# Performance work log

Hardware: AMD Instinct MI355X
Metric: run time of the kernel (lower is better)

## Reference

```python
import jax, jax.numpy as jnp
import numpy as np

B, D, V, T = 256, 1024, 32000, 64  # num_seqs, hidden dim, vocab, history len


def setup_inputs() -> dict:
    key = jax.random.key(0)
    ks = jax.random.split(key, 8)
    hidden = jax.random.normal(ks[0], (B, D), dtype=jnp.float32)
    embedding = jax.random.normal(ks[1], (V, D), dtype=jnp.float32) * (1.0 / np.sqrt(D))
    output_tokens = jax.random.randint(ks[2], (B, T), 0, V, dtype=jnp.int64)
    presence_penalties = jax.random.uniform(ks[3], (B,), dtype=jnp.float32)
    frequency_penalties = jax.random.uniform(ks[4], (B,), dtype=jnp.float32)
    temperatures = jax.random.uniform(ks[5], (B,), dtype=jnp.float32) + 0.5  # > eps
    top_ps = jax.random.uniform(ks[6], (B,), dtype=jnp.float32) * 0.5 + 0.5  # in [0.5, 1.0)
    top_ks = jax.random.randint(ks[7], (B,), 1, V, dtype=jnp.int64)
    return {
        "hidden": hidden,
        "embedding": embedding,
        "output_tokens": output_tokens,
        "presence_penalties": presence_penalties,
        "frequency_penalties": frequency_penalties,
        "temperatures": temperatures,
        "top_ps": top_ps,
        "top_ks": top_ks,
    }


def reference(hidden, embedding, output_tokens, presence_penalties,
              frequency_penalties, temperatures, top_ps, top_ks):
    # 1) logits = pruned hidden states @ embedding^T  -> [B, V]
    logits = jnp.einsum("bd,vd->bv", hidden, embedding)
    b, v = logits.shape

    # 2) presence/frequency penalties via per-row token histogram (np.bincount equiv)
    rows = jnp.broadcast_to(jnp.arange(b)[:, None], output_tokens.shape)
    counts = jnp.zeros((b, v), logits.dtype).at[rows, output_tokens].add(1.0)
    logits = logits - frequency_penalties[:, None] * counts \
                    - presence_penalties[:, None] * (counts > 0).astype(logits.dtype)

    # 3) temperature scaling
    logits = logits / temperatures[:, None]

    # 4) probabilities
    probs = jax.nn.softmax(logits, axis=-1)

    # 5) top-p / top-k: descending sort, cumsum masks, scatter back via inverse perm
    order = jnp.argsort(-probs, axis=-1)                       # descending order
    probs_sort = jnp.take_along_axis(probs, order, axis=-1)
    probs_cum = jnp.cumsum(probs_sort, axis=-1)
    top_p_mask = (probs_cum - probs_sort) > top_ps[:, None]
    top_k_mask = jnp.arange(v)[None, :] >= top_ks[:, None]
    probs_sort = jnp.where(top_p_mask | top_k_mask, 0.0, probs_sort)
    inv = jnp.argsort(order, axis=-1)
    filtered_probs = jnp.take_along_axis(probs_sort, inv, axis=-1)  # original order
    return filtered_probs
```

## Files before the change

### kernel.cpp

```cpp
#include <hip/hip_runtime.h>
#include <math.h>

#define NB 256
#define NV 32000
#define ND 1024
#define NT 64

#define GN 64
#define BSTR 40
#define NKB 64
#define AKBF 8192
#define NGBLK (NV / GN)
#define INV2048F 4.8828125e-4f

#define NBIN 1024
#define HSTR 1032
#define HTOT (4 * HSTR)
#define FIX2 4294967296.0
#define SMASK ((1ull << 48) - 1ull)

typedef _Float16 f16x8 __attribute__((ext_vector_type(8)));
typedef _Float16 f16x4 __attribute__((ext_vector_type(4)));
typedef float f32x16 __attribute__((ext_vector_type(16)));

struct RowP2 {
  unsigned long long basePack;
  unsigned long long toppZfix;
  unsigned pfx;
  int ktop;
  float invZ;
  unsigned ustar;
  int m;
  int cEq;
};

__device__ __forceinline__ unsigned mono_enc(float f) {
  unsigned u = __float_as_uint(f);
  return (u & 0x80000000u) ? ~u : (u | 0x80000000u);
}
__device__ __forceinline__ float mono_dec(unsigned u) {
  return (u & 0x80000000u) ? __uint_as_float(u & 0x7FFFFFFFu) : __uint_as_float(~u);
}

__global__ __launch_bounds__(256) void convert_A(const float* __restrict__ hidden,
                                                 _Float16* __restrict__ A3,
                                                 unsigned* __restrict__ rowmax) {
  if (blockIdx.x == 0) rowmax[threadIdx.x] = 0u;
  const int g = blockIdx.x * 256 + threadIdx.x;
  const int kb = g >> 10, rem = g & 1023, r = rem >> 2, c = rem & 3;
  const float4 a4 = *(const float4*)(hidden + (size_t)r * ND + kb * 16 + c * 4);
  const float v[4] = {a4.x, a4.y, a4.z, a4.w};
  f16x4 h4, q4;
#pragma unroll
  for (int q = 0; q < 4; q++) {
    const _Float16 hh = (_Float16)v[q];
    h4[q] = hh;
    q4[q] = (_Float16)((v[q] - (float)hh) * 2048.0f);
  }
  const int s = r >> 5, l31 = r & 31;
  const int lh = c >> 1, j4 = (c & 1) * 4;
  const int lane = l31 + (lh << 5);
  _Float16* base = A3 + (size_t)kb * AKBF;
  *(f16x4*)(base + ((s * 2 + 0) * 64 + lane) * 8 + j4) = h4;
  *(f16x4*)(base + ((s * 2 + 1) * 64 + lane) * 8 + j4) = q4;
}

__global__ __launch_bounds__(256, 2) void gemm_f16s(
    const float* __restrict__ Bm, const _Float16* __restrict__ A3,
    const float* __restrict__ temp, unsigned* __restrict__ rowmax,
    float* __restrict__ C) {
  __shared__ _Float16 Bls[2][GN * BSTR];
  __shared__ float s_invT[256];
  __shared__ unsigned s_pm[256];

  const int t = threadIdx.x;
  const int l = t & 63, w = t >> 6;
  const int n0 = blockIdx.x * GN;
  s_invT[t] = 1.0f / temp[t];
  s_pm[t] = 0u;

  f32x16 accH[2][2] = {};
  f32x16 accC[2][2] = {};

  const int bn = t >> 2, bk4 = (t & 3) * 4;
  const int l31 = l & 31, lh = l >> 5;
  const int ka = lh * 8;
  const int mb = w * 64;

  const float* browp = Bm + (size_t)(n0 + bn) * ND + bk4;
  const _Float16* aB = A3 + 2048 * w + l * 8;

  f16x8 eh0, eh1, eq0, eq1;
  f16x8 oh0, oh1, oq0, oq1;

#define LOADA(P, KB)                                                  \
  do {                                                                \
    const _Float16* ap_ = aB + (size_t)(KB) * AKBF;                   \
    P##h0 = *(const f16x8*)(ap_);                                     \
    P##q0 = *(const f16x8*)(ap_ + 512);                               \
    P##h1 = *(const f16x8*)(ap_ + 1024);                              \
    P##q1 = *(const f16x8*)(ap_ + 1536);                              \
  } while (0)

#define BCONV(BV, DST)                                                \
  do {                                                                \
    f16x4 h4_, q4_;                                                   \
    const float vv_[4] = {(BV).x, (BV).y, (BV).z, (BV).w};            \
    _Pragma("unroll") for (int j_ = 0; j_ < 4; j_++) {                \
      const _Float16 h_ = (_Float16)vv_[j_];                          \
      h4_[j_] = h_;                                                   \
      q4_[j_] = (_Float16)((vv_[j_] - (float)h_) * 2048.0f);          \
    }                                                                 \
    _Float16* prow_ = (DST) + bn * BSTR;                              \
    *(f16x4*)(prow_ + bk4) = h4_;                                     \
    *(f16x4*)(prow_ + 16 + bk4) = q4_;                                \
  } while (0)

#define COMPUTE(P, CUR)                                                                     \
  do {                                                                                      \
    const _Float16* Bp_ = &Bls[CUR][0] + (size_t)l31 * BSTR + ka;                           \
    f16x8 b0h_ = *(const f16x8*)(Bp_);                                                      \
    f16x8 b1h_ = *(const f16x8*)(Bp_ + 32 * BSTR);                                          \
    accH[0][0] = __builtin_amdgcn_mfma_f32_32x32x16_f16(P##h0, b0h_, accH[0][0], 0, 0, 0);  \
    accH[0][1] = __builtin_amdgcn_mfma_f32_32x32x16_f16(P##h0, b1h_, accH[0][1], 0, 0, 0);  \
    accH[1][0] = __builtin_amdgcn_mfma_f32_32x32x16_f16(P##h1, b0h_, accH[1][0], 0, 0, 0);  \
    accH[1][1] = __builtin_amdgcn_mfma_f32_32x32x16_f16(P##h1, b1h_, accH[1][1], 0, 0, 0);  \
    f16x8 b0q_ = *(const f16x8*)(Bp_ + 16);                                                 \
    f16x8 b1q_ = *(const f16x8*)(Bp_ + 32 * BSTR + 16);                                     \
    accC[0][0] = __builtin_amdgcn_mfma_f32_32x32x16_f16(P##h0, b0q_, accC[0][0], 0, 0, 0);  \
    accC[0][1] = __builtin_amdgcn_mfma_f32_32x32x16_f16(P##h0, b1q_, accC[0][1], 0, 0, 0);  \
    accC[1][0] = __builtin_amdgcn_mfma_f32_32x32x16_f16(P##h1, b0q_, accC[1][0], 0, 0, 0);  \
    accC[1][1] = __builtin_amdgcn_mfma_f32_32x32x16_f16(P##h1, b1q_, accC[1][1], 0, 0, 0);  \
    accC[0][0] = __builtin_amdgcn_mfma_f32_32x32x16_f16(P##q0, b0h_, accC[0][0], 0, 0, 0);  \
    accC[0][1] = __builtin_amdgcn_mfma_f32_32x32x16_f16(P##q0, b1h_, accC[0][1], 0, 0, 0);  \
    accC[1][0] = __builtin_amdgcn_mfma_f32_32x32x16_f16(P##q1, b0h_, accC[1][0], 0, 0, 0);  \
    accC[1][1] = __builtin_amdgcn_mfma_f32_32x32x16_f16(P##q1, b1h_, accC[1][1], 0, 0, 0);  \
  } while (0)

  LOADA(e, 0);
  __builtin_amdgcn_sched_barrier(0);
  float4 bv0 = *(const float4*)(browp);
  __builtin_amdgcn_sched_barrier(0);
  LOADA(o, 1);
  __builtin_amdgcn_sched_barrier(0);
  float4 bvA = *(const float4*)(browp + 16);
  __builtin_amdgcn_sched_barrier(0);
  BCONV(bv0, &Bls[0][0]);
  asm volatile("s_waitcnt lgkmcnt(0)\ns_barrier" ::: "memory");

  float4 bvB;
  for (int kb = 0; kb < 62; kb += 2) {
    COMPUTE(e, 0);
    __builtin_amdgcn_sched_barrier(0);
    LOADA(e, kb + 2);
    __builtin_amdgcn_sched_barrier(0);
    bvB = *(const float4*)(browp + (size_t)(kb + 2) * 16);
    __builtin_amdgcn_sched_barrier(0);
    BCONV(bvA, &Bls[1][0]);
    asm volatile("s_waitcnt lgkmcnt(0)\ns_barrier" ::: "memory");

    COMPUTE(o, 1);
    __builtin_amdgcn_sched_barrier(0);
    LOADA(o, kb + 3);
    __builtin_amdgcn_sched_barrier(0);
    bvA = *(const float4*)(browp + (size_t)(kb + 3) * 16);
    __builtin_amdgcn_sched_barrier(0);
    BCONV(bvB, &Bls[0][0]);
    asm volatile("s_waitcnt lgkmcnt(0)\ns_barrier" ::: "memory");
  }
  COMPUTE(e, 0);
  __builtin_amdgcn_sched_barrier(0);
  BCONV(bvA, &Bls[1][0]);
  asm volatile("s_waitcnt lgkmcnt(0)\ns_barrier" ::: "memory");
  COMPUTE(o, 1);

#undef LOADA
#undef BCONV
#undef COMPUTE

#pragma unroll
  for (int mi = 0; mi < 2; mi++) {
#pragma unroll
    for (int r = 0; r < 16; r++) {
      const int row = mb + mi * 32 + (r & 3) + 8 * (r >> 2) + 4 * lh;
      const float it = s_invT[row];
      float v0 = (accH[mi][0][r] + accC[mi][0][r] * INV2048F) * it;
      float v1 = (accH[mi][1][r] + accC[mi][1][r] * INV2048F) * it;
      C[(size_t)row * NV + n0 + l31] = v0;
      C[(size_t)row * NV + n0 + 32 + l31] = v1;
      float mx = fmaxf(v0, v1);
#pragma unroll
      for (int o = 1; o < 32; o <<= 1) mx = fmaxf(mx, __shfl_xor(mx, o));
      if (l31 == 0) atomicMax(&s_pm[row], mono_enc(mx));
    }
  }
  __syncthreads();
  atomicMax(&rowmax[t], s_pm[t]);
}

__global__ __launch_bounds__(1024) void sample_row(
    float* __restrict__ buf, const unsigned* __restrict__ rowmax,
    const int* __restrict__ toks, const float* __restrict__ pres,
    const float* __restrict__ freq, const float* __restrict__ temp,
    const float* __restrict__ topp_a, const int* __restrict__ topk_a) {
  __shared__ unsigned hist[HTOT];
  unsigned long long* suf = (unsigned long long*)hist;
  __shared__ unsigned long long wtot16[16];
  __shared__ int s_tok[NT];
  __shared__ int s_bs;
  __shared__ RowP2 sp;

  const int b = blockIdx.x, t = threadIdx.x;
  const int cp = (t >> 6) & 1;
  unsigned* loP = hist + cp * HSTR;
  unsigned* hcP = hist + 2 * HSTR + cp * HSTR;
  float* row = buf + (size_t)b * NV;

#define HACC(K, BIN)                                                            \
  do {                                                                          \
    unsigned long long m_ = (unsigned long long)(((K) & 0x7FFFFFu) | 0x800000u);\
    const int sh_ = (int)((K) >> 23) - 118;                                     \
    const unsigned long long f_ =                                               \
        (sh_ >= 0) ? (m_ << sh_) : ((sh_ > -24) ? (m_ >> (-sh_)) : 0ull);       \
    const unsigned flo_ = (unsigned)f_;                                         \
    const unsigned old_ = atomicAdd(&loP[BIN], flo_);                           \
    const unsigned hc_ = 0x10000u + (unsigned)(f_ >> 32) +                      \
                         ((old_ + flo_ < flo_) ? 1u : 0u);                      \
    atomicAdd(&hcP[BIN], hc_);                                                  \
  } while (0)

  if (t < NT) s_tok[t] = toks[b * NT + t];
  for (int i = t; i < HTOT; i += 1024) hist[i] = 0u;
  __syncthreads();

  if (t < NT) {
    const int tk = s_tok[t];
    bool first = true; int cnt = 0;
    for (int j = 0; j < NT; j++)
      if (s_tok[j] == tk) { if (j < t) first = false; cnt++; }
    if (first) row[tk] -= (freq[b] * (float)cnt + pres[b]) / temp[b];
  }
  __syncthreads();

  const float M = mono_dec(rowmax[b]);
  for (int i4 = t; i4 < NV / 4; i4 += 1024) {
    float4 x4 = *(const float4*)(row + i4 * 4);
    float4 e4;
    e4.x = expf(x4.x - M); e4.y = expf(x4.y - M);
    e4.z = expf(x4.z - M); e4.w = expf(x4.w - M);
    *(float4*)(row + i4 * 4) = e4;
    unsigned k;
    k = __float_as_uint(e4.x); if (k) HACC(k, k >> 20);
    k = __float_as_uint(e4.y); if (k) HACC(k, k >> 20);
    k = __float_as_uint(e4.z); if (k) HACC(k, k >> 20);
    k = __float_as_uint(e4.w); if (k) HACC(k, k >> 20);
  }
  __syncthreads();

  const int lane = t & 63, wv = t >> 6;
  for (int level = 0; level < 3; level++) {
    const unsigned lo0 = hist[t], lo1 = hist[HSTR + t];
    const unsigned hc0 = hist[2 * HSTR + t], hc1 = hist[3 * HSTR + t];
    const unsigned c = (hc0 >> 16) + (hc1 >> 16);
    const unsigned long long sum =
        (((unsigned long long)((hc0 & 0xFFFFu) + (hc1 & 0xFFFFu))) << 32) +
        (unsigned long long)lo0 + (unsigned long long)lo1;
    unsigned long long sv = ((unsigned long long)c << 48) + sum;
#pragma unroll
    for (int off = 1; off < 64; off <<= 1) {
      const unsigned long long up = __shfl_down(sv, off, 64);
      if (lane + off < 64) sv += up;
    }
    if (lane == 0) wtot16[wv] = sv;
    if (t == 0) s_bs = NBIN - 1;
    __syncthreads();
    unsigned long long add = 0ull, tot = 0ull;
#pragma unroll
    for (int w2 = 0; w2 < 16; w2++) {
      const unsigned long long x = wtot16[w2];
      tot += x;
      add += (w2 > wv) ? x : 0ull;
    }
    const unsigned long long mySuf = sv + add;
    suf[t] = mySuf;
    const unsigned long long totalP = tot;
    __syncthreads();

    unsigned long long base, toppZ;
    int ktop_;
    if (level == 0) {
      ktop_ = topk_a[b];
      unsigned long long Zfix = totalP & SMASK;
      if (!Zfix) Zfix = 1ull;
      toppZ = (unsigned long long)((double)topp_a[b] * (double)Zfix);
      base = 0ull;
    } else {
      base = sp.basePack; toppZ = sp.toppZfix; ktop_ = sp.ktop;
    }

    {
      const unsigned long long sG = base + mySuf;
      const bool A = ((long long)(sG >> 48) < (long long)ktop_) && ((sG & SMASK) <= toppZ);
      const unsigned long long sP = base + ((t > 0) ? suf[t - 1] : totalP);
      const bool Ap = ((long long)(sP >> 48) < (long long)ktop_) && ((sP & SMASK) <= toppZ);
      if (A && !Ap) s_bs = t;
    }
    __syncthreads();
    if (t == 0) {
      const int bs = s_bs;
      const unsigned long long newBase = base + suf[bs];
      if (level == 0) {
        unsigned long long Zfix = totalP & SMASK;
        if (!Zfix) Zfix = 1ull;
        sp.invZ = (float)(FIX2 / (double)Zfix);
      }
      if (level < 2) {
        sp.basePack = newBase;
        sp.toppZfix = toppZ;
        sp.ktop = ktop_;
        sp.pfx = (level == 0) ? (unsigned)bs : ((sp.pfx << 10) | (unsigned)bs);
      } else {
        const unsigned ustar = (sp.pfx << 10) | (unsigned)bs;
        const unsigned long long raw = ((bs > 0) ? suf[bs - 1] : totalP) - suf[bs];
        const int cEq = (int)(raw >> 48);
        const long long Chi = (long long)(newBase >> 48);
        const unsigned long long Shi = newBase & SMASK;
        long long m = cEq;
        const long long lim = (long long)ktop_ - Chi;
        if (lim < m) m = lim;
        const double tf = (double)__uint_as_float(ustar) * FIX2;
        const double rem = (double)(toppZ - Shi);
        const double Rd = floor(rem / tf) + 1.0;
        if (Rd < (double)m) m = (long long)Rd;
        if (m < 1) m = 1;
        sp.ustar = ustar; sp.m = (int)m; sp.cEq = cEq;
      }
    }
    __syncthreads();

    if (level < 2) {
      for (int i = t; i < HTOT; i += 1024) hist[i] = 0u;
      __syncthreads();
      const unsigned pfx = sp.pfx;
      const int ms = (level == 0) ? 20 : 10;
      const int bsh = (level == 0) ? 10 : 0;
      for (int i4 = t; i4 < NV / 4; i4 += 1024) {
        float4 e4 = *(const float4*)(row + i4 * 4);
        unsigned k;
        k = __float_as_uint(e4.x); if (k && (k >> ms) == pfx) HACC(k, (k >> bsh) & 1023u);
        k = __float_as_uint(e4.y); if (k && (k >> ms) == pfx) HACC(k, (k >> bsh) & 1023u);
        k = __float_as_uint(e4.z); if (k && (k >> ms) == pfx) HACC(k, (k >> bsh) & 1023u);
        k = __float_as_uint(e4.w); if (k && (k >> ms) == pfx) HACC(k, (k >> bsh) & 1023u);
      }
      __syncthreads();
    }
  }
#undef HACC

  const unsigned ustar = sp.ustar;
  const float invZ = sp.invZ;
  if (sp.m >= sp.cEq) {
    for (int i4 = t; i4 < NV / 4; i4 += 1024) {
      float4 e4 = *(const float4*)(row + i4 * 4);
      float4 o4;
      unsigned k;
      k = __float_as_uint(e4.x); o4.x = (k >= ustar) ? e4.x * invZ : 0.f;
      k = __float_as_uint(e4.y); o4.y = (k >= ustar) ? e4.y * invZ : 0.f;
      k = __float_as_uint(e4.z); o4.z = (k >= ustar) ? e4.z * invZ : 0.f;
      k = __float_as_uint(e4.w); o4.w = (k >= ustar) ? e4.w * invZ : 0.f;
      *(float4*)(row + i4 * 4) = o4;
    }
  } else {
    const int m = sp.m;
    unsigned* rk = hist;
    const int base0 = t * 32;
    const int end0 = (base0 + 32 < NV) ? base0 + 32 : NV;
    int myc = 0;
    for (int v = base0; v < end0; v++)
      myc += (__float_as_uint(row[v]) == ustar);
    rk[t] = (unsigned)myc;
    __syncthreads();
    for (int off = 1; off < 1024; off <<= 1) {
      const unsigned a0 = rk[t];
      const unsigned an = (t >= off) ? rk[t - off] : 0u;
      __syncthreads();
      rk[t] = a0 + an;
      __syncthreads();
    }
    int r = (t > 0) ? (int)rk[t - 1] : 0;
    for (int v = base0; v < end0; v++) {
      const unsigned k = __float_as_uint(row[v]);
      float o = (k > ustar) ? row[v] * invZ : 0.f;
      if (k == ustar) { o = (r < m) ? row[v] * invZ : 0.f; r++; }
      row[v] = o;
    }
  }
}

extern "C" void kernel_launch(void* const* d_in, const int* in_sizes, int n_in,
                              void* d_out, int out_size, void* d_ws, size_t ws_size,
                              hipStream_t stream) {
  (void)in_sizes; (void)n_in; (void)out_size; (void)ws_size;
  const float* hidden = (const float*)d_in[0];
  const float* emb    = (const float*)d_in[1];
  const int*   toks   = (const int*)d_in[2];
  const float* pres   = (const float*)d_in[3];
  const float* freq   = (const float*)d_in[4];
  const float* temp   = (const float*)d_in[5];
  const float* topp   = (const float*)d_in[6];
  const int*   topk   = (const int*)d_in[7];
  float* out = (float*)d_out;

  const size_t offA3 = 0;
  const size_t offRM = 1048576;

  _Float16* A3 = (_Float16*)((char*)d_ws + offA3);
  unsigned* rowmax = (unsigned*)((char*)d_ws + offRM);

  convert_A<<<256, 256, 0, stream>>>(hidden, A3, rowmax);
  gemm_f16s<<<NGBLK, 256, 0, stream>>>(emb, A3, temp, rowmax, out);
  sample_row<<<NB, 1024, 0, stream>>>(out, rowmax, toks, pres, freq,
                                      temp, topp, topk);
}
```

Baseline: 276.6 us.

## Load embedding fragments directly into registers, drop LDS staging and barriers

The GEMM no longer stages converted embedding tiles through shared memory with per-step barriers. Each lane now loads its own B fragment from global memory as float4s and splits it into fp16 hi/lo parts in registers right before the MFMAs. This removes LDS traffic and block-wide barriers from the main loop. In exchange each of the four waves loads and converts the same B data separately, which multiplies global/L2 loads and conversion ALU work by four and raises register pressure.

```diff
diff --git a/kernel.cpp b/kernel.cpp
--- a/kernel.cpp
+++ b/kernel.cpp
@@ -7,7 +7,6 @@
 #define NT 64
 
 #define GN 64
-#define BSTR 40
 #define NKB 64
 #define AKBF 8192
 #define NGBLK (NV / GN)
@@ -69,7 +68,6 @@
     const float* __restrict__ Bm, const _Float16* __restrict__ A3,
     const float* __restrict__ temp, unsigned* __restrict__ rowmax,
     float* __restrict__ C) {
-  __shared__ _Float16 Bls[2][GN * BSTR];
   __shared__ float s_invT[256];
   __shared__ unsigned s_pm[256];
 
@@ -78,20 +76,23 @@
   const int n0 = blockIdx.x * GN;
   s_invT[t] = 1.0f / temp[t];
   s_pm[t] = 0u;
+  __syncthreads();
 
   f32x16 accH[2][2] = {};
   f32x16 accC[2][2] = {};
 
-  const int bn = t >> 2, bk4 = (t & 3) * 4;
   const int l31 = l & 31, lh = l >> 5;
   const int ka = lh * 8;
   const int mb = w * 64;
 
-  const float* browp = Bm + (size_t)(n0 + bn) * ND + bk4;
+  const float* b0p = Bm + (size_t)(n0 + l31) * ND + ka;
+  const float* b1p = Bm + (size_t)(n0 + 32 + l31) * ND + ka;
   const _Float16* aB = A3 + 2048 * w + l * 8;
 
   f16x8 eh0, eh1, eq0, eq1;
   f16x8 oh0, oh1, oq0, oq1;
+  float4 ebf0a, ebf0b, ebf1a, ebf1b;
+  float4 obf0a, obf0b, obf1a, obf1b;
 
 #define LOADA(P, KB)                                                  \
   do {                                                                \
@@ -102,31 +103,35 @@
     P##q1 = *(const f16x8*)(ap_ + 1536);                              \
   } while (0)
 
-#define BCONV(BV, DST)                                                \
+#define LOADB(P, KB)                                                  \
   do {                                                                \
-    f16x4 h4_, q4_;                                                   \
-    const float vv_[4] = {(BV).x, (BV).y, (BV).z, (BV).w};            \
-    _Pragma("unroll") for (int j_ = 0; j_ < 4; j_++) {                \
-      const _Float16 h_ = (_Float16)vv_[j_];                          \
-      h4_[j_] = h_;                                                   \
-      q4_[j_] = (_Float16)((vv_[j_] - (float)h_) * 2048.0f);          \
-    }                                                                 \
-    _Float16* prow_ = (DST) + bn * BSTR;                              \
-    *(f16x4*)(prow_ + bk4) = h4_;                                     \
-    *(f16x4*)(prow_ + 16 + bk4) = q4_;                                \
+    const float* p0_ = b0p + (size_t)(KB) * 16;                       \
+    const float* p1_ = b1p + (size_t)(KB) * 16;                       \
+    P##bf0a = *(const float4*)(p0_);                                  \
+    P##bf0b = *(const float4*)(p0_ + 4);                              \
+    P##bf1a = *(const float4*)(p1_);                                  \
+    P##bf1b = *(const float4*)(p1_ + 4);                              \
   } while (0)
 
-#define COMPUTE(P, CUR)                                                                     \
+#define COMPUTE(P)                                                                          \
   do {                                                                                      \
-    const _Float16* Bp_ = &Bls[CUR][0] + (size_t)l31 * BSTR + ka;                           \
-    f16x8 b0h_ = *(const f16x8*)(Bp_);                                                      \
-    f16x8 b1h_ = *(const f16x8*)(Bp_ + 32 * BSTR);                                          \
+    const float s0_[8] = {P##bf0a.x, P##bf0a.y, P##bf0a.z, P##bf0a.w,                       \
+                          P##bf0b.x, P##bf0b.y, P##bf0b.z, P##bf0b.w};                      \
+    const float s1_[8] = {P##bf1a.x, P##bf1a.y, P##bf1a.z, P##bf1a.w,                       \
+                          P##bf1b.x, P##bf1b.y, P##bf1b.z, P##bf1b.w};                      \
+    f16x8 b0h_, b0q_, b1h_, b1q_;                                                           \
+    _Pragma("unroll") for (int j_ = 0; j_ < 8; j_++) {                                      \
+      const _Float16 h0_ = (_Float16)s0_[j_];                                               \
+      b0h_[j_] = h0_;                                                                       \
+      b0q_[j_] = (_Float16)((s0_[j_] - (float)h0_) * 2048.0f);                              \
+      const _Float16 h1_ = (_Float16)s1_[j_];                                               \
+      b1h_[j_] = h1_;                                                                       \
+      b1q_[j_] = (_Float16)((s1_[j_] - (float)h1_) * 2048.0f);                              \
+    }                                                                                       \
     accH[0][0] = __builtin_amdgcn_mfma_f32_32x32x16_f16(P##h0, b0h_, accH[0][0], 0, 0, 0);  \
     accH[0][1] = __builtin_amdgcn_mfma_f32_32x32x16_f16(P##h0, b1h_, accH[0][1], 0, 0, 0);  \
     accH[1][0] = __builtin_amdgcn_mfma_f32_32x32x16_f16(P##h1, b0h_, accH[1][0], 0, 0, 0);  \
     accH[1][1] = __builtin_amdgcn_mfma_f32_32x32x16_f16(P##h1, b1h_, accH[1][1], 0, 0, 0);  \
-    f16x8 b0q_ = *(const f16x8*)(Bp_ + 16);                                                 \
-    f16x8 b1q_ = *(const f16x8*)(Bp_ + 32 * BSTR + 16);                                     \
     accC[0][0] = __builtin_amdgcn_mfma_f32_32x32x16_f16(P##h0, b0q_, accC[0][0], 0, 0, 0);  \
     accC[0][1] = __builtin_amdgcn_mfma_f32_32x32x16_f16(P##h0, b1q_, accC[0][1], 0, 0, 0);  \
     accC[1][0] = __builtin_amdgcn_mfma_f32_32x32x16_f16(P##h1, b0q_, accC[1][0], 0, 0, 0);  \
@@ -137,45 +142,27 @@
     accC[1][1] = __builtin_amdgcn_mfma_f32_32x32x16_f16(P##q1, b1h_, accC[1][1], 0, 0, 0);  \
   } while (0)
 
-  LOADA(e, 0);
+  LOADA(e, 0); LOADB(e, 0);
   __builtin_amdgcn_sched_barrier(0);
-  float4 bv0 = *(const float4*)(browp);
+  LOADA(o, 1); LOADB(o, 1);
   __builtin_amdgcn_sched_barrier(0);
-  LOADA(o, 1);
+
+  for (int kb = 0; kb < 62; kb += 2) {
+    COMPUTE(e);
+    __builtin_amdgcn_sched_barrier(0);
+    LOADA(e, kb + 2); LOADB(e, kb + 2);
+    __builtin_amdgcn_sched_barrier(0);
+    COMPUTE(o);
+    __builtin_amdgcn_sched_barrier(0);
+    LOADA(o, kb + 3); LOADB(o, kb + 3);
+    __builtin_amdgcn_sched_barrier(0);
+  }
+  COMPUTE(e);
   __builtin_amdgcn_sched_barrier(0);
-  float4 bvA = *(const float4*)(browp + 16);
-  __builtin_amdgcn_sched_barrier(0);
-  BCONV(bv0, &Bls[0][0]);
-  asm volatile("s_waitcnt lgkmcnt(0)\ns_barrier" ::: "memory");
-
-  float4 bvB;
-  for (int kb = 0; kb < 62; kb += 2) {
-    COMPUTE(e, 0);
-    __builtin_amdgcn_sched_barrier(0);
-    LOADA(e, kb + 2);
-    __builtin_amdgcn_sched_barrier(0);
-    bvB = *(const float4*)(browp + (size_t)(kb + 2) * 16);
-    __builtin_amdgcn_sched_barrier(0);
-    BCONV(bvA, &Bls[1][0]);
-    asm volatile("s_waitcnt lgkmcnt(0)\ns_barrier" ::: "memory");
-
-    COMPUTE(o, 1);
-    __builtin_amdgcn_sched_barrier(0);
-    LOADA(o, kb + 3);
-    __builtin_amdgcn_sched_barrier(0);
-    bvA = *(const float4*)(browp + (size_t)(kb + 3) * 16);
-    __builtin_amdgcn_sched_barrier(0);
-    BCONV(bvB, &Bls[0][0]);
-    asm volatile("s_waitcnt lgkmcnt(0)\ns_barrier" ::: "memory");
-  }
-  COMPUTE(e, 0);
-  __builtin_amdgcn_sched_barrier(0);
-  BCONV(bvA, &Bls[1][0]);
-  asm volatile("s_waitcnt lgkmcnt(0)\ns_barrier" ::: "memory");
-  COMPUTE(o, 1);
+  COMPUTE(o);
 
 #undef LOADA
-#undef BCONV
+#undef LOADB
 #undef COMPUTE
 
 #pragma unroll
```

Result: slower. 307.7 us (+11.3%).

## Split final filter pass into separate wide-grid kernels with tie-handling kernel

Applied to the files above, without the earlier changes.

The per-row sampling kernel now only computes the selection parameters and writes them to workspace. The final masking and scaling pass runs in a separate kernel over 8 blocks per row, which spreads the memory-bound write across more of the GPU. Elements equal to the threshold are marked by negating them when tie-breaking is needed. A third kernel then resolves those ties with a prefix count. This adds two kernel launches and an extra read/write pass, and the tie kernel does a serial scan over each row.

```diff
diff --git a/kernel.cpp b/kernel.cpp
--- a/kernel.cpp
+++ b/kernel.cpp
@@ -198,11 +198,12 @@
   atomicMax(&rowmax[t], s_pm[t]);
 }
 
-__global__ __launch_bounds__(1024) void sample_row(
+__global__ __launch_bounds__(1024) void sample_select(
     float* __restrict__ buf, const unsigned* __restrict__ rowmax,
     const int* __restrict__ toks, const float* __restrict__ pres,
     const float* __restrict__ freq, const float* __restrict__ temp,
-    const float* __restrict__ topp_a, const int* __restrict__ topk_a) {
+    const float* __restrict__ topp_a, const int* __restrict__ topk_a,
+    RowP2* __restrict__ params) {
   __shared__ unsigned hist[HTOT];
   unsigned long long* suf = (unsigned long long*)hist;
   __shared__ unsigned long long wtot16[16];
@@ -334,6 +335,7 @@
         if (Rd < (double)m) m = (long long)Rd;
         if (m < 1) m = 1;
         sp.ustar = ustar; sp.m = (int)m; sp.cEq = cEq;
+        params[b] = sp;
       }
     }
     __syncthreads();
@@ -356,43 +358,65 @@
     }
   }
 #undef HACC
-
-  const unsigned ustar = sp.ustar;
-  const float invZ = sp.invZ;
-  if (sp.m >= sp.cEq) {
-    for (int i4 = t; i4 < NV / 4; i4 += 1024) {
-      float4 e4 = *(const float4*)(row + i4 * 4);
+}
+
+__global__ __launch_bounds__(256) void s3_filter(
+    float* __restrict__ buf, const RowP2* __restrict__ params) {
+  const int b = blockIdx.x >> 3, sl = blockIdx.x & 7, t = threadIdx.x;
+  const RowP2 p = params[b];
+  const unsigned ustar = p.ustar;
+  const float invZ = p.invZ;
+  const bool need = (p.m < p.cEq);
+  float* row = buf + (size_t)b * NV;
+  const int base = sl * 4096;
+#pragma unroll
+  for (int it = 0; it < 4; it++) {
+    const int idx = base + (it * 256 + t) * 4;
+    if (idx < NV) {
+      float4 e4 = *(const float4*)(row + idx);
       float4 o4;
       unsigned k;
-      k = __float_as_uint(e4.x); o4.x = (k >= ustar) ? e4.x * invZ : 0.f;
-      k = __float_as_uint(e4.y); o4.y = (k >= ustar) ? e4.y * invZ : 0.f;
-      k = __float_as_uint(e4.z); o4.z = (k >= ustar) ? e4.z * invZ : 0.f;
-      k = __float_as_uint(e4.w); o4.w = (k >= ustar) ? e4.w * invZ : 0.f;
-      *(float4*)(row + i4 * 4) = o4;
-    }
-  } else {
-    const int m = sp.m;
-    unsigned* rk = hist;
-    const int base0 = t * 32;
-    const int end0 = (base0 + 32 < NV) ? base0 + 32 : NV;
-    int myc = 0;
-    for (int v = base0; v < end0; v++)
-      myc += (__float_as_uint(row[v]) == ustar);
-    rk[t] = (unsigned)myc;
-    __syncthreads();
-    for (int off = 1; off < 1024; off <<= 1) {
-      const unsigned a0 = rk[t];
-      const unsigned an = (t >= off) ? rk[t - off] : 0u;
-      __syncthreads();
-      rk[t] = a0 + an;
-      __syncthreads();
-    }
-    int r = (t > 0) ? (int)rk[t - 1] : 0;
-    for (int v = base0; v < end0; v++) {
-      const unsigned k = __float_as_uint(row[v]);
-      float o = (k > ustar) ? row[v] * invZ : 0.f;
-      if (k == ustar) { o = (r < m) ? row[v] * invZ : 0.f; r++; }
-      row[v] = o;
+      k = __float_as_uint(e4.x);
+      o4.x = (k > ustar) ? e4.x * invZ : ((k == ustar) ? (need ? -e4.x : e4.x * invZ) : 0.f);
+      k = __float_as_uint(e4.y);
+      o4.y = (k > ustar) ? e4.y * invZ : ((k == ustar) ? (need ? -e4.y : e4.y * invZ) : 0.f);
+      k = __float_as_uint(e4.z);
+      o4.z = (k > ustar) ? e4.z * invZ : ((k == ustar) ? (need ? -e4.z : e4.z * invZ) : 0.f);
+      k = __float_as_uint(e4.w);
+      o4.w = (k > ustar) ? e4.w * invZ : ((k == ustar) ? (need ? -e4.w : e4.w * invZ) : 0.f);
+      *(float4*)(row + idx) = o4;
+    }
+  }
+}
+
+__global__ __launch_bounds__(256) void s5_tie(
+    float* __restrict__ buf, const RowP2* __restrict__ params) {
+  const int b = blockIdx.x, t = threadIdx.x;
+  const RowP2 p = params[b];
+  if (p.m >= p.cEq) return;
+  const int m = p.m;
+  const float invZ = p.invZ;
+  float* row = buf + (size_t)b * NV;
+  __shared__ int s_rank[256];
+  const int CH = NV / 256;
+  const int base = t * CH, end = base + CH;
+  int myc = 0;
+  for (int v = base; v < end; v++) myc += (row[v] < 0.f);
+  s_rank[t] = myc;
+  __syncthreads();
+  for (int off = 1; off < 256; off <<= 1) {
+    const int v0 = s_rank[t];
+    const int vn = (t >= off) ? s_rank[t - off] : 0;
+    __syncthreads();
+    s_rank[t] = v0 + vn;
+    __syncthreads();
+  }
+  int r = (t > 0) ? s_rank[t - 1] : 0;
+  for (int v = base; v < end; v++) {
+    const float f = row[v];
+    if (f < 0.f) {
+      row[v] = (r < m) ? (-f) * invZ : 0.f;
+      r++;
     }
   }
 }
@@ -411,14 +435,18 @@
   const int*   topk   = (const int*)d_in[7];
   float* out = (float*)d_out;
 
-  const size_t offA3 = 0;
-  const size_t offRM = 1048576;
+  const size_t offA3  = 0;
+  const size_t offRM  = 1048576;
+  const size_t offPar = offRM + 1024;
 
   _Float16* A3 = (_Float16*)((char*)d_ws + offA3);
   unsigned* rowmax = (unsigned*)((char*)d_ws + offRM);
+  RowP2* params = (RowP2*)((char*)d_ws + offPar);
 
   convert_A<<<256, 256, 0, stream>>>(hidden, A3, rowmax);
   gemm_f16s<<<NGBLK, 256, 0, stream>>>(emb, A3, temp, rowmax, out);
-  sample_row<<<NB, 1024, 0, stream>>>(out, rowmax, toks, pres, freq,
-                                      temp, topp, topk);
-}
+  sample_select<<<NB, 1024, 0, stream>>>(out, rowmax, toks, pres, freq,
+                                         temp, topp, topk, params);
+  s3_filter<<<NB * 8, 256, 0, stream>>>(out, params);
+  s5_tie<<<NB, 256, 0, stream>>>(out, params);
+}
```

After: 277.2 us. No clear change (+0.2%).
